# Performance work log

Hardware: AMD Instinct MI355X
Metric: run time of the kernel (lower is better)

Reference implementation:

```python
import jax, jax.numpy as jnp
import numpy as np

N = 4096          # n_nodes
M = 8192          # m_nodes (= 2*N, required by block structure)
D = 128           # in_dim == hidden_dim (conv1 is reapplied to its own output)
H = 128
NUM_ITERS = 3


def setup_inputs() -> dict:
    key = jax.random.key(0)
    ks = jax.random.split(key, 6)
    X = jax.random.normal(ks[0], (N, D), dtype=jnp.float32)
    R = jax.random.uniform(ks[1], (N, N), dtype=jnp.float32)
    A = 0.5 * (R + R.T)  # symmetric, strictly positive connectivity matrix
    # upsample MLP: Linear(n_nodes -> m_nodes - n_nodes), torch weight layout [out, in]
    W_up = jax.random.normal(ks[2], (M - N, N), dtype=jnp.float32) * 0.02
    b_up = jnp.zeros((M - N,), dtype=jnp.float32)
    # GCNConv linear weights stored [in, out]
    W1 = jax.random.normal(ks[3], (D, H), dtype=jnp.float32) * 0.05
    b1 = jnp.zeros((H,), dtype=jnp.float32)
    W2 = jax.random.normal(ks[4], (H, H), dtype=jnp.float32) * 0.05
    b2 = jnp.zeros((H,), dtype=jnp.float32)
    return dict(X=X, A=A, W_up=W_up, b_up=b_up, W1=W1, b1=b1, W2=W2, b2=b2)


def _gcn(Adj, X, W, b):
    # PyG GCNConv on a fully dense, strictly-positive weighted graph:
    # every diagonal entry is nonzero, so add_remaining_self_loops is a no-op and
    # out = D^{-1/2} A D^{-1/2} (X W) + b  exactly.
    deg = Adj.sum(axis=0)                         # [m] column degree
    dinv = jnp.where(deg > 0, jax.lax.rsqrt(deg), 0.0)
    An = Adj * dinv[:, None] * dinv[None, :]      # symmetric normalization
    return An @ (X @ W) + b


def reference(X, A, W_up, b_up, W1, b1, W2, b2):
    # new_nodes = upsample_mlp(X.T).T  -> [M-N, D]
    new_nodes = (X.T @ W_up.T + b_up).T
    Xu = jnp.concatenate([X, new_nodes], axis=0)  # [M, D]
    # block adjacency: [[A, A.T], [A, sigmoid(new @ new.T)]]
    Adj = jnp.block([[A, A.T],
                     [A, jax.nn.sigmoid(new_nodes @ new_nodes.T)]])  # [M, M]
    A_out = Adj
    for _ in range(NUM_ITERS):
        Xu = jax.nn.relu(_gcn(Adj, Xu, W1, b1))
        Adj = jax.nn.sigmoid(Xu @ Xu.T)           # mid-loop adjacency rebuild
        Xu = jax.nn.relu(_gcn(Adj, Xu, W2, b2))
        A_out = jax.nn.sigmoid(Xu @ Xu.T)
        # NOTE: edge_index for the next conv1 is NOT rebuilt from A_out in the
        # original (only after conv1), so Adj carries the mid-loop matrix.
    return A_out
```

## Files before the change

kernel.cpp:

```cpp
#include <hip/hip_runtime.h>
#include <hip/hip_bf16.h>


#define N_NODES 4096
#define M_NODES 8192
#define DIM 128
#define SLICE_ELEMS ((size_t)M_NODES * DIM)

typedef __attribute__((ext_vector_type(4))) float f32x4;
typedef __attribute__((ext_vector_type(8))) short bf16x8;

__device__ __forceinline__ unsigned short f2bf(float f) {
  union { float f; unsigned u; } v; v.f = f;
  unsigned r = v.u + 0x7fffu + ((v.u >> 16) & 1u);
  return (unsigned short)(r >> 16);
}

__device__ __forceinline__ void gld16(unsigned short* lds, const unsigned short* g) {
  __builtin_amdgcn_global_load_lds(
      (const __attribute__((address_space(1))) unsigned int*)g,
      (__attribute__((address_space(3))) unsigned int*)lds, 16, 0, 0);
}

__device__ __forceinline__ float sigmoidf_(float x) { return 1.0f / (1.0f + __expf(-x)); }


__global__ void cast_x_kernel(const float* __restrict__ X, unsigned short* __restrict__ Xu,
                              unsigned short* __restrict__ XT,
                              const float* __restrict__ W1, const float* __restrict__ W2,
                              unsigned short* __restrict__ W1T,
                              unsigned short* __restrict__ W2T,
                              float* __restrict__ deg) {
  int idx = blockIdx.x * 256 + threadIdx.x;
  if (idx < M_NODES) deg[idx] = 0.f;
  if (idx < 32768) {
    const float* W = idx < 16384 ? W1 : W2;
    unsigned short* WT = idx < 16384 ? W1T : W2T;
    int j = idx & 16383;
    int k = j >> 7, c = j & 127;
    WT[c * DIM + k] = f2bf(W[j]);
  }
  int i = idx >> 7, c = idx & 127;
  unsigned short b = f2bf(X[idx]);
  Xu[idx] = b;
  XT[(size_t)c * N_NODES + i] = b;
}

__global__ void cast_a_kernel(const float* __restrict__ A, unsigned short* __restrict__ Adj,
                              float* __restrict__ deg) {
  int c = blockIdx.x * 256 + threadIdx.x;
  int r0 = blockIdx.y * 128;
  int tm = r0 >> 7;
  int kc = c >> 10, st = (c & 1023) >> 5, e = c & 31;
  size_t a1 = ((size_t)(tm)      * 8 + kc)     * 131072 + (size_t)st * 4096 + e;
  size_t a2 = ((size_t)(tm)      * 8 + 4 + kc) * 131072 + (size_t)st * 4096 + e;
  size_t a3 = ((size_t)(tm + 32) * 8 + kc)     * 131072 + (size_t)st * 4096 + e;
  float s = 0.f;
  for (int r = 0; r < 128; ++r) {
    float a = A[(size_t)(r0 + r) * N_NODES + c];
    unsigned short b = f2bf(a);
    Adj[a1 + r * 32] = b; Adj[a2 + r * 32] = b; Adj[a3 + r * 32] = b;
    s += a;
  }
  atomicAdd(&deg[c], 2.0f * s);
  atomicAdd(&deg[N_NODES + c], s);
}


__global__ __launch_bounds__(256, 2)
void agg64_kernel(const unsigned short* __restrict__ At,
                  const unsigned short* __restrict__ BT, long ldb,
                  float* __restrict__ accBase, int kIters) {
  __shared__ __align__(16) unsigned short smem[18432];
  const int t = threadIdx.x, w = t >> 6, lane = t & 63;
  const int q = lane >> 4, l15 = lane & 15;
  const int sx = (l15 >> 1) & 3;
  const int wm = w & 1, wn = w >> 1;
  const int tm = blockIdx.x >> 1;
  const int h2048 = (blockIdx.x & 1) * 2048;
  const int sg0 = blockIdx.y * kIters;
  const int arow = t >> 2;
  const int xchk = (t & 3) ^ ((t >> 3) & 3);

  auto STAGE = [&](int s, int b) {
    unsigned short* la = smem + b * 6144;
    unsigned short* lb = la + 2048;
    int sg = sg0 + s;
    size_t aaddr = ((size_t)tm * 8 + (sg >> 5)) * 131072 + (size_t)(sg & 31) * 4096 + h2048;
    gld16(&la[t * 8],        &At[aaddr + arow * 32 + xchk * 8]);
    gld16(&lb[t * 8],        &BT[(size_t)arow * ldb + (size_t)sg * 32 + xchk * 8]);
    gld16(&lb[2048 + t * 8], &BT[(size_t)(64 + arow) * ldb + (size_t)sg * 32 + xchk * 8]);
  };

  f32x4 acc[2][4];
#pragma unroll
  for (int a = 0; a < 2; ++a)
#pragma unroll
    for (int b = 0; b < 4; ++b) acc[a][b] = (f32x4)0.f;

  STAGE(0, 0);
  STAGE(1, 1);

  for (int s = 0; s < kIters; ++s) {
    if (s + 2 < kIters) {
      STAGE(s + 2, (s + 2) % 3);
      asm volatile("s_waitcnt vmcnt(6)" ::: "memory");
    } else if (s + 1 < kIters) {
      asm volatile("s_waitcnt vmcnt(3)" ::: "memory");
    } else {
      asm volatile("s_waitcnt vmcnt(0)" ::: "memory");
    }
    __builtin_amdgcn_s_barrier();
    __builtin_amdgcn_sched_barrier(0);

    const unsigned short* la = smem + (s % 3) * 6144;
    const unsigned short* lb = la + 2048;
    bf16x8 a0 = *(const bf16x8*)&la[(wm * 32 + l15) * 32 + (q ^ sx) * 8];
    bf16x8 a1 = *(const bf16x8*)&la[(wm * 32 + 16 + l15) * 32 + (q ^ sx) * 8];
#pragma unroll
    for (int nt = 0; nt < 4; ++nt) {
      bf16x8 b = *(const bf16x8*)&lb[(wn * 64 + nt * 16 + l15) * 32 + (q ^ sx) * 8];
      acc[0][nt] = __builtin_amdgcn_mfma_f32_16x16x32_bf16(a0, b, acc[0][nt], 0, 0, 0);
      acc[1][nt] = __builtin_amdgcn_mfma_f32_16x16x32_bf16(a1, b, acc[1][nt], 0, 0, 0);
    }
    __builtin_amdgcn_sched_barrier(0);
    __builtin_amdgcn_s_barrier();
    __builtin_amdgcn_sched_barrier(0);
  }
  float* ct = accBase + (size_t)blockIdx.y * SLICE_ELEMS + (size_t)blockIdx.x * 8192;
#pragma unroll
  for (int mt = 0; mt < 2; ++mt)
#pragma unroll
    for (int nt = 0; nt < 4; ++nt)
      *(f32x4*)&ct[((w * 8 + mt * 4 + nt) * 256) + (q * 16 + l15) * 4] = acc[mt][nt];
}


__global__ __launch_bounds__(256)
void up_agg_f32(const float* __restrict__ Wup, const unsigned short* __restrict__ BT,
                float* __restrict__ accBase) {
  __shared__ __align__(16) unsigned short smem[6144];
  unsigned short* la = smem;
  unsigned short* lb = smem + 2048;
  const int t = threadIdx.x, w = t >> 6, lane = t & 63;
  const int q = lane >> 4, l15 = lane & 15;
  const int r0 = blockIdx.x * 64;
  const int k0 = blockIdx.y * 512;
  const int arow = t >> 2, achk = t & 3;

  f32x4 acc[8];
#pragma unroll
  for (int b = 0; b < 8; ++b) acc[b] = (f32x4)0.f;

  for (int s = 0; s < 16; ++s) {
    int kb = k0 + s * 32;
    __syncthreads();
    gld16(&lb[t * 8],        &BT[(size_t)arow * N_NODES + kb + achk * 8]);
    gld16(&lb[2048 + t * 8], &BT[(size_t)(64 + arow) * N_NODES + kb + achk * 8]);
    const float* ap = &Wup[(size_t)(r0 + (t >> 2)) * N_NODES + kb + (t & 3) * 8];
    float4 v0 = *(const float4*)ap;
    float4 v1 = *(const float4*)(ap + 4);
    ushort4 o0, o1;
    o0.x = f2bf(v0.x); o0.y = f2bf(v0.y); o0.z = f2bf(v0.z); o0.w = f2bf(v0.w);
    o1.x = f2bf(v1.x); o1.y = f2bf(v1.y); o1.z = f2bf(v1.z); o1.w = f2bf(v1.w);
    *(ushort4*)&la[t * 8] = o0;
    *(ushort4*)&la[t * 8 + 4] = o1;
    __syncthreads();

    bf16x8 a0 = *(const bf16x8*)&la[(w * 16 + l15) * 32 + q * 8];
#pragma unroll
    for (int nt = 0; nt < 8; ++nt) {
      bf16x8 b = *(const bf16x8*)&lb[(nt * 16 + l15) * 32 + q * 8];
      acc[nt] = __builtin_amdgcn_mfma_f32_16x16x32_bf16(a0, b, acc[nt], 0, 0, 0);
    }
  }
  float* ct = accBase + (size_t)blockIdx.y * SLICE_ELEMS + (size_t)blockIdx.x * 8192;
#pragma unroll
  for (int nt = 0; nt < 8; ++nt)
    *(f32x4*)&ct[((w * 8 + nt) * 256) + (q * 16 + l15) * 4] = acc[nt];
}

__global__ void reduce64_kernel(const float* __restrict__ acc,
                                unsigned short* __restrict__ dst,
                                const float* __restrict__ bias_row,
                                const float* __restrict__ bias_col,
                                const float* __restrict__ deg, int mode, int nSlices) {
  int p = blockIdx.x * 256 + threadIdx.x;
  float s = 0.f;
  for (int sp = 0; sp < nSlices; ++sp) s += acc[(size_t)sp * SLICE_ELEMS + p];
  int tile = p >> 13, r = p & 8191;
  int grp = r >> 8;
  int r2 = r & 255;
  int i = r2 & 3, ql = r2 >> 2;
  int row, col;
  float v;
  if (mode == 0) {
    int w = grp >> 3, nt = grp & 7;
    row = tile * 64 + w * 16 + (ql >> 4) * 4 + i;
    col = nt * 16 + (ql & 15);
    v = s + bias_row[row];
  } else {
    int w = grp >> 3, mt = (grp >> 2) & 1, nt = grp & 3;
    row = tile * 64 + (w & 1) * 32 + mt * 16 + (ql >> 4) * 4 + i;
    col = (w >> 1) * 64 + nt * 16 + (ql & 15);
    float d = deg[row];
    float dv = d > 0.f ? rsqrtf(d) : 0.f;
    v = fmaxf(dv * s + bias_col[col], 0.f);
  }
  dst[(size_t)row * DIM + col] = f2bf(v);
}


template <int MODE>
__global__ __launch_bounds__(256)
void rebuild_kernel(const unsigned short* __restrict__ XA,
                    const unsigned short* __restrict__ XB,
                    void* __restrict__ out, long p1 ,
                    long col0, float* __restrict__ deg, int nB) {
  __shared__ __align__(16) unsigned short smem[34816];
  __shared__ float lcol[128];
  __shared__ float lrow[128];
  unsigned short* lA = smem;
  unsigned short* lB = smem + 16384;
  const int t = threadIdx.x, w = t >> 6, lane = t & 63;
  const int q = lane >> 4, l15 = lane & 15;
  const int sx = (l15 >> 1) & 3;

  int rem = blockIdx.x, bi = 0;
  while (rem >= nB - bi) { rem -= nB - bi; ++bi; }
  const int bj = bi + rem;
  const int i0 = bi * 128, j0 = bj * 128;
  const bool offdiag = (bi != bj);

  const int srow = t >> 2;
  const int xchk = (t & 3) ^ ((t >> 3) & 3);
#pragma unroll
  for (int kk = 0; kk < 4; ++kk)
#pragma unroll
    for (int h = 0; h < 2; ++h) {
      gld16(&lA[kk * 4096 + h * 2048 + t * 8],
            &XA[(size_t)(i0 + h * 64 + srow) * DIM + kk * 32 + xchk * 8]);
      gld16(&lB[kk * 4096 + h * 2048 + t * 8],
            &XB[(size_t)(j0 + h * 64 + srow) * DIM + kk * 32 + xchk * 8]);
    }
  if (MODE == 0 && t < 128) { lcol[t] = 0.f; lrow[t] = 0.f; }
  __syncthreads();

  f32x4 acc[2][8];
#pragma unroll
  for (int a = 0; a < 2; ++a)
#pragma unroll
    for (int b = 0; b < 8; ++b) acc[a][b] = (f32x4)0.f;

#pragma unroll
  for (int kk = 0; kk < 4; ++kk) {
    bf16x8 a0 = *(const bf16x8*)&lA[kk * 4096 + (w * 32 + l15) * 32 + ((q ^ sx)) * 8];
    bf16x8 a1 = *(const bf16x8*)&lA[kk * 4096 + (w * 32 + 16 + l15) * 32 + ((q ^ sx)) * 8];
#pragma unroll
    for (int nt = 0; nt < 8; ++nt) {
      bf16x8 b = *(const bf16x8*)&lB[kk * 4096 + (nt * 16 + l15) * 32 + ((q ^ sx)) * 8];
      acc[0][nt] = __builtin_amdgcn_mfma_f32_16x16x32_bf16(a0, b, acc[0][nt], 0, 0, 0);
      acc[1][nt] = __builtin_amdgcn_mfma_f32_16x16x32_bf16(a1, b, acc[1][nt], 0, 0, 0);
    }
  }
  __syncthreads();

  if (MODE == 0) {
    unsigned short* lC  = smem;
    unsigned short* lCt = smem + 17408;
    float rs[2][4] = {{0.f, 0.f, 0.f, 0.f}, {0.f, 0.f, 0.f, 0.f}};
#pragma unroll
    for (int mt = 0; mt < 2; ++mt)
#pragma unroll
      for (int nt = 0; nt < 8; ++nt) {
        float cs = 0.f;
#pragma unroll
        for (int i = 0; i < 4; ++i) {
          float sv = sigmoidf_(acc[mt][nt][i]);
          cs += sv;
          unsigned short hb = f2bf(sv);
          int row = w * 32 + mt * 16 + q * 4 + i, colL = nt * 16 + l15;
          lC[row * 136 + colL] = hb;
          if (offdiag) { lCt[colL * 136 + row] = hb; rs[mt][i] += sv; }
        }
        cs += __shfl_xor(cs, 16);
        cs += __shfl_xor(cs, 32);
        if (lane < 16) atomicAdd(&lcol[nt * 16 + lane], cs);
      }
    if (offdiag) {
#pragma unroll
      for (int mt = 0; mt < 2; ++mt)
#pragma unroll
        for (int i = 0; i < 4; ++i) {
          float v = rs[mt][i];
          v += __shfl_xor(v, 1); v += __shfl_xor(v, 2);
          v += __shfl_xor(v, 4); v += __shfl_xor(v, 8);
          if (l15 == 0) atomicAdd(&lrow[w * 32 + mt * 16 + q * 4 + i], v);
        }
    }
    __syncthreads();
    unsigned short* og = (unsigned short*)out;
    {
      const long rowbase = p1 + i0, colbase = col0 + j0;
      const size_t tb = ((size_t)(rowbase >> 7) * 8 + (colbase >> 10)) * 131072;
      const int stb = (int)((colbase & 1023) >> 5);
#pragma unroll
      for (int cc = 0; cc < 8; ++cc) {
        int ch = t + cc * 256;
        int row = ch >> 4, c16 = ch & 15;
        *(bf16x8*)&og[tb + (size_t)(stb + (c16 >> 2)) * 4096 + row * 32 + (c16 & 3) * 8] =
            *(const bf16x8*)&lC[row * 136 + c16 * 8];
      }
    }
    if (offdiag) {
      const long rowbase = p1 + j0, colbase = col0 + i0;
      const size_t tb = ((size_t)(rowbase >> 7) * 8 + (colbase >> 10)) * 131072;
      const int stb = (int)((colbase & 1023) >> 5);
#pragma unroll
      for (int cc = 0; cc < 8; ++cc) {
        int ch = t + cc * 256;
        int row = ch >> 4, c16 = ch & 15;
        *(bf16x8*)&og[tb + (size_t)(stb + (c16 >> 2)) * 4096 + row * 32 + (c16 & 3) * 8] =
            *(const bf16x8*)&lCt[row * 136 + c16 * 8];
      }
    }
    if (t < 128) atomicAdd(&deg[col0 + j0 + t], lcol[t]);
    if (offdiag && t < 128) atomicAdd(&deg[col0 + i0 + t], lrow[t]);
  } else {
    float* og = (float*)out;
    float* lCf = (float*)smem;
#pragma unroll
    for (int mt = 0; mt < 2; ++mt)
#pragma unroll
      for (int nt = 0; nt < 8; ++nt)
#pragma unroll
        for (int i = 0; i < 4; ++i) acc[mt][nt][i] = sigmoidf_(acc[mt][nt][i]);
#pragma unroll
    for (int h2 = 0; h2 < 2; ++h2) {
      __syncthreads();
      if ((w >> 1) == h2) {
#pragma unroll
        for (int mt = 0; mt < 2; ++mt)
#pragma unroll
          for (int nt = 0; nt < 8; ++nt)
#pragma unroll
            for (int i = 0; i < 4; ++i)
              lCf[((w & 1) * 32 + mt * 16 + q * 4 + i) * 132 + nt * 16 + l15] =
                  acc[mt][nt][i];
      }
      __syncthreads();
#pragma unroll
      for (int j = 0; j < 8; ++j) {
        int ch = t + j * 256;
        int r64 = ch >> 5, c4 = (ch & 31) * 4;
        *(f32x4*)&og[(size_t)(i0 + h2 * 64 + r64) * p1 + j0 + c4] =
            *(const f32x4*)&lCf[r64 * 132 + c4];
      }
    }
    if (offdiag) {
#pragma unroll
      for (int h2 = 0; h2 < 2; ++h2) {
        __syncthreads();
#pragma unroll
        for (int mt = 0; mt < 2; ++mt)
#pragma unroll
          for (int nt = 0; nt < 8; ++nt)
            if ((nt >> 2) == h2) {
#pragma unroll
              for (int i = 0; i < 4; ++i)
                lCf[((nt & 3) * 16 + l15) * 132 + (w * 32 + mt * 16 + q * 4 + i)] =
                    acc[mt][nt][i];
            }
        __syncthreads();
#pragma unroll
        for (int j = 0; j < 8; ++j) {
          int ch = t + j * 256;
          int r64 = ch >> 5, c4 = (ch & 31) * 4;
          *(f32x4*)&og[(size_t)(j0 + h2 * 64 + r64) * p1 + i0 + c4] =
              *(const f32x4*)&lCf[r64 * 132 + c4];
        }
      }
    }
  }
}


__global__ __launch_bounds__(256)
void yz_kernel(const unsigned short* __restrict__ Xu, const unsigned short* __restrict__ WT,
               const float* __restrict__ deg, unsigned short* __restrict__ ZT, int ldz,
               float* __restrict__ zbuf) {
  __shared__ __align__(16) unsigned short smem[32768];
  unsigned short* lA = smem;
  unsigned short* lB = smem + 16384;
  const int t = threadIdx.x, w = t >> 6, lane = t & 63;
  const int q = lane >> 4, l15 = lane & 15;
  const int sx = (l15 >> 1) & 3;
  const int r0 = blockIdx.x * 128;
  if (zbuf) {
    int gid = blockIdx.x * 256 + t;
    if (gid < M_NODES) zbuf[gid] = 0.f;
  }
  const int srow = t >> 2;
  const int xchk = (t & 3) ^ ((t >> 3) & 3);
#pragma unroll
  for (int kk = 0; kk < 4; ++kk)
#pragma unroll
    for (int h = 0; h < 2; ++h) {
      gld16(&lA[kk * 4096 + h * 2048 + t * 8],
            &Xu[(size_t)(r0 + h * 64 + srow) * DIM + kk * 32 + xchk * 8]);
      gld16(&lB[kk * 4096 + h * 2048 + t * 8],
            &WT[(size_t)(h * 64 + srow) * DIM + kk * 32 + xchk * 8]);
    }
  __syncthreads();

  f32x4 acc[2][8];
#pragma unroll
  for (int a = 0; a < 2; ++a)
#pragma unroll
    for (int b = 0; b < 8; ++b) acc[a][b] = (f32x4)0.f;

#pragma unroll
  for (int kk = 0; kk < 4; ++kk) {
    bf16x8 a0 = *(const bf16x8*)&lA[kk * 4096 + (w * 32 + l15) * 32 + (q ^ sx) * 8];
    bf16x8 a1 = *(const bf16x8*)&lA[kk * 4096 + (w * 32 + 16 + l15) * 32 + (q ^ sx) * 8];
#pragma unroll
    for (int nt = 0; nt < 8; ++nt) {
      bf16x8 b = *(const bf16x8*)&lB[kk * 4096 + (nt * 16 + l15) * 32 + (q ^ sx) * 8];
      acc[0][nt] = __builtin_amdgcn_mfma_f32_16x16x32_bf16(a0, b, acc[0][nt], 0, 0, 0);
      acc[1][nt] = __builtin_amdgcn_mfma_f32_16x16x32_bf16(a1, b, acc[1][nt], 0, 0, 0);
    }
  }
  __syncthreads();
  unsigned short* lT = smem;
#pragma unroll
  for (int mt = 0; mt < 2; ++mt)
#pragma unroll
    for (int i = 0; i < 4; ++i) {
      int r = w * 32 + mt * 16 + q * 4 + i;
      float d = deg[r0 + r];
      float dv = d > 0.f ? rsqrtf(d) : 0.f;
#pragma unroll
      for (int nt = 0; nt < 8; ++nt)
        lT[(nt * 16 + l15) * 136 + r] = f2bf(dv * acc[mt][nt][i]);
    }
  __syncthreads();
#pragma unroll
  for (int cc = 0; cc < 8; ++cc) {
    int ch = t + cc * 256;
    int c = ch >> 4, c16 = ch & 15;
    *(bf16x8*)&ZT[(size_t)c * ldz + r0 + c16 * 8] = *(const bf16x8*)&lT[c * 136 + c16 * 8];
  }
}


extern "C" void kernel_launch(void* const* d_in, const int* in_sizes, int n_in,
                              void* d_out, int out_size, void* d_ws, size_t ws_size,
                              hipStream_t stream) {
  (void)in_sizes; (void)n_in; (void)out_size;
  const float* X   = (const float*)d_in[0];
  const float* A   = (const float*)d_in[1];
  const float* Wup = (const float*)d_in[2];
  const float* bup = (const float*)d_in[3];
  const float* W1  = (const float*)d_in[4];
  const float* b1  = (const float*)d_in[5];
  const float* W2  = (const float*)d_in[6];
  const float* b2  = (const float*)d_in[7];

  const size_t ADJ_BYTES = (size_t)M_NODES * M_NODES * 2;
  char* ws = (char*)d_ws;
  size_t off = 0;
  auto alloc = [&](size_t bytes) {
    char* p = ws + off;
    off += (bytes + 255) & ~(size_t)255;
    return p;
  };
  float*          accb    = (float*)alloc(8 * SLICE_ELEMS * 4);
  unsigned short* Xu      = (unsigned short*)alloc((size_t)M_NODES * DIM * 2);
  unsigned short* ZT      = (unsigned short*)alloc((size_t)DIM * M_NODES * 2);
  unsigned short* XT      = (unsigned short*)alloc((size_t)DIM * N_NODES * 2);
  unsigned short* W1T     = (unsigned short*)alloc(DIM * DIM * 2);
  unsigned short* W2T     = (unsigned short*)alloc(DIM * DIM * 2);
  float*          degA    = (float*)alloc(M_NODES * 4);
  float*          degB    = (float*)alloc(M_NODES * 4);

  unsigned short* Adj;
  if (ws_size >= off + ADJ_BYTES) Adj = (unsigned short*)(ws + off);
  else                            Adj = (unsigned short*)d_out;

  unsigned short* XuNew = Xu + (size_t)N_NODES * DIM;

  cast_x_kernel<<<N_NODES * DIM / 256, 256, 0, stream>>>(X, Xu, XT, W1, W2, W1T, W2T, degA);

  up_agg_f32<<<dim3(N_NODES / 64, 8), 256, 0, stream>>>(Wup, XT, accb);
  reduce64_kernel<<<N_NODES * DIM / 256, 256, 0, stream>>>(
      accb, XuNew, bup, nullptr, nullptr, 0, 8);

  cast_a_kernel<<<dim3(N_NODES / 256, N_NODES / 128), 256, 0, stream>>>(A, Adj, degA);
  rebuild_kernel<0><<<32 * 33 / 2, 256, 0, stream>>>(
      XuNew, XuNew, Adj, N_NODES, N_NODES, degA, 32);

  float* degCur = degA;
  float* degMid = degB;
  for (int it = 0; it < 3; ++it) {
    yz_kernel<<<M_NODES / 128, 256, 0, stream>>>(Xu, W1T, degCur, ZT, M_NODES, degMid);
    agg64_kernel<<<dim3(M_NODES / 64, 4), 256, 0, stream>>>(Adj, ZT, M_NODES, accb, 64);
    reduce64_kernel<<<M_NODES * DIM / 256, 256, 0, stream>>>(
        accb, Xu, nullptr, b1, degCur, 1, 4);
    rebuild_kernel<0><<<64 * 65 / 2, 256, 0, stream>>>(
        Xu, Xu, Adj, 0, 0, degMid, 64);
    yz_kernel<<<M_NODES / 128, 256, 0, stream>>>(Xu, W2T, degMid, ZT, M_NODES, nullptr);
    agg64_kernel<<<dim3(M_NODES / 64, 4), 256, 0, stream>>>(Adj, ZT, M_NODES, accb, 64);
    reduce64_kernel<<<M_NODES * DIM / 256, 256, 0, stream>>>(
        accb, Xu, nullptr, b2, degMid, 1, 4);
    if (it == 2)
      rebuild_kernel<1><<<64 * 65 / 2, 256, 0, stream>>>(
          Xu, Xu, d_out, M_NODES, 0, nullptr, 64);
    float* tmp = degCur; degCur = degMid; degMid = tmp;
  }
}
```

Before: 893.7 us.

## Store adjacency as 8-bit e5m2 and aggregate with f16 MFMA

The 8192x8192 adjacency is stored as 1-byte e5m2 (truncated fp16) instead of bf16, halving its memory footprint and traffic in the rebuild and aggregation kernels. The aggregation kernel is rewritten to load 64-wide K chunks of fp8 A, expand them to fp16 in registers with byte permutes, and feed f16 MFMAs, with ZT now produced in fp16. Degree sums are computed from the quantized values so the normalization stays consistent with them. The cost is a large precision drop for adjacency values (2 mantissa bits), which risks accuracy tolerance, plus extra ALU work to expand the bytes.

```diff
diff --git a/kernel.cpp b/kernel.cpp
--- a/kernel.cpp
+++ b/kernel.cpp
@@ -9,6 +9,7 @@
 
 typedef __attribute__((ext_vector_type(4))) float f32x4;
 typedef __attribute__((ext_vector_type(8))) short bf16x8;
+typedef __attribute__((ext_vector_type(8))) _Float16 half8;
 
 __device__ __forceinline__ unsigned short f2bf(float f) {
   union { float f; unsigned u; } v; v.f = f;
@@ -16,13 +17,44 @@
   return (unsigned short)(r >> 16);
 }
 
+__device__ __forceinline__ unsigned short f2h(float f) {
+  union { _Float16 h; unsigned short u; } v; v.h = (_Float16)f; return v.u;
+}
+
+__device__ __forceinline__ unsigned char f2e5(float f) {
+  unsigned short h = f2h(f);
+  unsigned short r = h + 0x7Fu + ((h >> 8) & 1u);
+  return (unsigned char)(r >> 8);
+}
+__device__ __forceinline__ float e5tof(unsigned char b) {
+  union { unsigned short u; _Float16 h; } v; v.u = (unsigned short)b << 8;
+  return (float)v.h;
+}
+
 __device__ __forceinline__ void gld16(unsigned short* lds, const unsigned short* g) {
   __builtin_amdgcn_global_load_lds(
       (const __attribute__((address_space(1))) unsigned int*)g,
       (__attribute__((address_space(3))) unsigned int*)lds, 16, 0, 0);
 }
+__device__ __forceinline__ void gld16b(unsigned char* lds, const unsigned char* g) {
+  __builtin_amdgcn_global_load_lds(
+      (const __attribute__((address_space(1))) unsigned int*)g,
+      (__attribute__((address_space(3))) unsigned int*)lds, 16, 0, 0);
+}
 
 __device__ __forceinline__ float sigmoidf_(float x) { return 1.0f / (1.0f + __expf(-x)); }
+
+__device__ __forceinline__ half8 expandA(const unsigned char* la, int row, int c16, int hf) {
+  const unsigned* p =
+      (const unsigned*)&la[(((c16 ^ (row & 3)) * 64 + row) * 16) + hf * 8];
+  unsigned x0 = p[0], x1 = p[1];
+  union { unsigned u[4]; half8 h; } r;
+  r.u[0] = __builtin_amdgcn_perm(x0, 0u, 0x050C040Cu);
+  r.u[1] = __builtin_amdgcn_perm(x0, 0u, 0x070C060Cu);
+  r.u[2] = __builtin_amdgcn_perm(x1, 0u, 0x050C040Cu);
+  r.u[3] = __builtin_amdgcn_perm(x1, 0u, 0x070C060Cu);
+  return r.h;
+}
 
 
 __global__ void cast_x_kernel(const float* __restrict__ X, unsigned short* __restrict__ Xu,
@@ -46,7 +78,7 @@
   XT[(size_t)c * N_NODES + i] = b;
 }
 
-__global__ void cast_a_kernel(const float* __restrict__ A, unsigned short* __restrict__ Adj,
+__global__ void cast_a_kernel(const float* __restrict__ A, unsigned char* __restrict__ Adj,
                               float* __restrict__ deg) {
   int c = blockIdx.x * 256 + threadIdx.x;
   int r0 = blockIdx.y * 128;
@@ -58,9 +90,9 @@
   float s = 0.f;
   for (int r = 0; r < 128; ++r) {
     float a = A[(size_t)(r0 + r) * N_NODES + c];
-    unsigned short b = f2bf(a);
+    unsigned char b = f2e5(a);
     Adj[a1 + r * 32] = b; Adj[a2 + r * 32] = b; Adj[a3 + r * 32] = b;
-    s += a;
+    s += e5tof(b);
   }
   atomicAdd(&deg[c], 2.0f * s);
   atomicAdd(&deg[N_NODES + c], s);
@@ -68,28 +100,34 @@
 
 
 __global__ __launch_bounds__(256, 2)
-void agg64_kernel(const unsigned short* __restrict__ At,
+void aggf8_kernel(const unsigned char* __restrict__ At,
                   const unsigned short* __restrict__ BT, long ldb,
-                  float* __restrict__ accBase, int kIters) {
-  __shared__ __align__(16) unsigned short smem[18432];
+                  float* __restrict__ accBase) {
+  __shared__ __align__(16) unsigned char smem[61440];
   const int t = threadIdx.x, w = t >> 6, lane = t & 63;
   const int q = lane >> 4, l15 = lane & 15;
-  const int sx = (l15 >> 1) & 3;
   const int wm = w & 1, wn = w >> 1;
   const int tm = blockIdx.x >> 1;
-  const int h2048 = (blockIdx.x & 1) * 2048;
-  const int sg0 = blockIdx.y * kIters;
-  const int arow = t >> 2;
-  const int xchk = (t & 3) ^ ((t >> 3) & 3);
+  const int hrow = (blockIdx.x & 1) * 64;
+  const int sg0 = blockIdx.y * 64;
+  const int arow = lane;
+  const int ac16 = w ^ (lane & 3);
 
   auto STAGE = [&](int s, int b) {
-    unsigned short* la = smem + b * 6144;
-    unsigned short* lb = la + 2048;
-    int sg = sg0 + s;
-    size_t aaddr = ((size_t)tm * 8 + (sg >> 5)) * 131072 + (size_t)(sg & 31) * 4096 + h2048;
-    gld16(&la[t * 8],        &At[aaddr + arow * 32 + xchk * 8]);
-    gld16(&lb[t * 8],        &BT[(size_t)arow * ldb + (size_t)sg * 32 + xchk * 8]);
-    gld16(&lb[2048 + t * 8], &BT[(size_t)(64 + arow) * ldb + (size_t)sg * 32 + xchk * 8]);
+    unsigned char* la = smem + b * 20480;
+    unsigned short* lb = (unsigned short*)(la + 4096);
+    int sg = sg0 + 2 * s + (ac16 >> 1);
+    gld16b(&la[t * 16],
+           &At[((size_t)tm * 8 + (sg >> 5)) * 131072 + (size_t)(sg & 31) * 4096 +
+               (hrow + arow) * 32 + (ac16 & 1) * 16]);
+    size_t kb = (size_t)sg0 * 32 + (size_t)s * 64;
+#pragma unroll
+    for (int j = 0; j < 4; ++j) {
+      int ch = j * 256 + t;
+      int row = ch >> 3, phys = ch & 7;
+      int c = phys ^ (row & 7);
+      gld16(&lb[ch * 8], &BT[(size_t)row * ldb + kb + c * 8]);
+    }
   };
 
   f32x4 acc[2][4];
@@ -101,27 +139,33 @@
   STAGE(0, 0);
   STAGE(1, 1);
 
-  for (int s = 0; s < kIters; ++s) {
-    if (s + 2 < kIters) {
+  for (int s = 0; s < 32; ++s) {
+    if (s + 2 < 32) {
       STAGE(s + 2, (s + 2) % 3);
-      asm volatile("s_waitcnt vmcnt(6)" ::: "memory");
-    } else if (s + 1 < kIters) {
-      asm volatile("s_waitcnt vmcnt(3)" ::: "memory");
+      asm volatile("s_waitcnt vmcnt(10)" ::: "memory");
+    } else if (s + 1 < 32) {
+      asm volatile("s_waitcnt vmcnt(5)" ::: "memory");
     } else {
       asm volatile("s_waitcnt vmcnt(0)" ::: "memory");
     }
     __builtin_amdgcn_s_barrier();
     __builtin_amdgcn_sched_barrier(0);
 
-    const unsigned short* la = smem + (s % 3) * 6144;
-    const unsigned short* lb = la + 2048;
-    bf16x8 a0 = *(const bf16x8*)&la[(wm * 32 + l15) * 32 + (q ^ sx) * 8];
-    bf16x8 a1 = *(const bf16x8*)&la[(wm * 32 + 16 + l15) * 32 + (q ^ sx) * 8];
-#pragma unroll
-    for (int nt = 0; nt < 4; ++nt) {
-      bf16x8 b = *(const bf16x8*)&lb[(wn * 64 + nt * 16 + l15) * 32 + (q ^ sx) * 8];
-      acc[0][nt] = __builtin_amdgcn_mfma_f32_16x16x32_bf16(a0, b, acc[0][nt], 0, 0, 0);
-      acc[1][nt] = __builtin_amdgcn_mfma_f32_16x16x32_bf16(a1, b, acc[1][nt], 0, 0, 0);
+    const unsigned char* la = smem + (s % 3) * 20480;
+    const unsigned short* lb = (const unsigned short*)(la + 4096);
+#pragma unroll
+    for (int kk = 0; kk < 2; ++kk) {
+      int ch8 = kk * 4 + q;
+      int c16 = ch8 >> 1, hf = ch8 & 1;
+      half8 a0 = expandA(la, wm * 32 + l15, c16, hf);
+      half8 a1 = expandA(la, wm * 32 + 16 + l15, c16, hf);
+#pragma unroll
+      for (int nt = 0; nt < 4; ++nt) {
+        int brow = wn * 64 + nt * 16 + l15;
+        half8 b = *(const half8*)&lb[brow * 64 + (ch8 ^ (l15 & 7)) * 8];
+        acc[0][nt] = __builtin_amdgcn_mfma_f32_16x16x32_f16(a0, b, acc[0][nt], 0, 0, 0);
+        acc[1][nt] = __builtin_amdgcn_mfma_f32_16x16x32_f16(a1, b, acc[1][nt], 0, 0, 0);
+      }
     }
     __builtin_amdgcn_sched_barrier(0);
     __builtin_amdgcn_s_barrier();
@@ -266,8 +310,8 @@
   __syncthreads();
 
   if (MODE == 0) {
-    unsigned short* lC  = smem;
-    unsigned short* lCt = smem + 17408;
+    unsigned char* lC  = (unsigned char*)smem;
+    unsigned char* lCt = (unsigned char*)smem + 17408;
     float rs[2][4] = {{0.f, 0.f, 0.f, 0.f}, {0.f, 0.f, 0.f, 0.f}};
 #pragma unroll
     for (int mt = 0; mt < 2; ++mt)
@@ -276,12 +320,12 @@
         float cs = 0.f;
 #pragma unroll
         for (int i = 0; i < 4; ++i) {
-          float sv = sigmoidf_(acc[mt][nt][i]);
-          cs += sv;
-          unsigned short hb = f2bf(sv);
+          unsigned char hb = f2e5(sigmoidf_(acc[mt][nt][i]));
+          float dq = e5tof(hb);
+          cs += dq;
           int row = w * 32 + mt * 16 + q * 4 + i, colL = nt * 16 + l15;
           lC[row * 136 + colL] = hb;
-          if (offdiag) { lCt[colL * 136 + row] = hb; rs[mt][i] += sv; }
+          if (offdiag) { lCt[colL * 136 + row] = hb; rs[mt][i] += dq; }
         }
         cs += __shfl_xor(cs, 16);
         cs += __shfl_xor(cs, 32);
@@ -299,7 +343,7 @@
         }
     }
     __syncthreads();
-    unsigned short* og = (unsigned short*)out;
+    unsigned char* og = (unsigned char*)out;
     {
       const long rowbase = p1 + i0, colbase = col0 + j0;
       const size_t tb = ((size_t)(rowbase >> 7) * 8 + (colbase >> 10)) * 131072;
@@ -308,8 +352,9 @@
       for (int cc = 0; cc < 8; ++cc) {
         int ch = t + cc * 256;
         int row = ch >> 4, c16 = ch & 15;
-        *(bf16x8*)&og[tb + (size_t)(stb + (c16 >> 2)) * 4096 + row * 32 + (c16 & 3) * 8] =
-            *(const bf16x8*)&lC[row * 136 + c16 * 8];
+        *(unsigned long long*)
+            &og[tb + (size_t)(stb + (c16 >> 2)) * 4096 + row * 32 + (c16 & 3) * 8] =
+            *(const unsigned long long*)&lC[row * 136 + c16 * 8];
       }
     }
     if (offdiag) {
@@ -320,8 +365,9 @@
       for (int cc = 0; cc < 8; ++cc) {
         int ch = t + cc * 256;
         int row = ch >> 4, c16 = ch & 15;
-        *(bf16x8*)&og[tb + (size_t)(stb + (c16 >> 2)) * 4096 + row * 32 + (c16 & 3) * 8] =
-            *(const bf16x8*)&lCt[row * 136 + c16 * 8];
+        *(unsigned long long*)
+            &og[tb + (size_t)(stb + (c16 >> 2)) * 4096 + row * 32 + (c16 & 3) * 8] =
+            *(const unsigned long long*)&lCt[row * 136 + c16 * 8];
       }
     }
     if (t < 128) atomicAdd(&deg[col0 + j0 + t], lcol[t]);
@@ -441,7 +487,7 @@
       float dv = d > 0.f ? rsqrtf(d) : 0.f;
 #pragma unroll
       for (int nt = 0; nt < 8; ++nt)
-        lT[(nt * 16 + l15) * 136 + r] = f2bf(dv * acc[mt][nt][i]);
+        lT[(nt * 16 + l15) * 136 + r] = f2h(dv * acc[mt][nt][i]);
     }
   __syncthreads();
 #pragma unroll
@@ -466,7 +512,7 @@
   const float* W2  = (const float*)d_in[6];
   const float* b2  = (const float*)d_in[7];
 
-  const size_t ADJ_BYTES = (size_t)M_NODES * M_NODES * 2;
+  const size_t ADJ_BYTES = (size_t)M_NODES * M_NODES;
   char* ws = (char*)d_ws;
   size_t off = 0;
   auto alloc = [&](size_t bytes) {
@@ -483,9 +529,9 @@
   float*          degA    = (float*)alloc(M_NODES * 4);
   float*          degB    = (float*)alloc(M_NODES * 4);
 
-  unsigned short* Adj;
-  if (ws_size >= off + ADJ_BYTES) Adj = (unsigned short*)(ws + off);
-  else                            Adj = (unsigned short*)d_out;
+  unsigned char* Adj;
+  if (ws_size >= off + ADJ_BYTES) Adj = (unsigned char*)(ws + off);
+  else                            Adj = (unsigned char*)d_out;
 
   unsigned short* XuNew = Xu + (size_t)N_NODES * DIM;
 
@@ -503,13 +549,13 @@
   float* degMid = degB;
   for (int it = 0; it < 3; ++it) {
     yz_kernel<<<M_NODES / 128, 256, 0, stream>>>(Xu, W1T, degCur, ZT, M_NODES, degMid);
-    agg64_kernel<<<dim3(M_NODES / 64, 4), 256, 0, stream>>>(Adj, ZT, M_NODES, accb, 64);
+    aggf8_kernel<<<dim3(M_NODES / 64, 4), 256, 0, stream>>>(Adj, ZT, M_NODES, accb);
     reduce64_kernel<<<M_NODES * DIM / 256, 256, 0, stream>>>(
         accb, Xu, nullptr, b1, degCur, 1, 4);
     rebuild_kernel<0><<<64 * 65 / 2, 256, 0, stream>>>(
         Xu, Xu, Adj, 0, 0, degMid, 64);
     yz_kernel<<<M_NODES / 128, 256, 0, stream>>>(Xu, W2T, degMid, ZT, M_NODES, nullptr);
-    agg64_kernel<<<dim3(M_NODES / 64, 4), 256, 0, stream>>>(Adj, ZT, M_NODES, accb, 64);
+    aggf8_kernel<<<dim3(M_NODES / 64, 4), 256, 0, stream>>>(Adj, ZT, M_NODES, accb);
     reduce64_kernel<<<M_NODES * DIM / 256, 256, 0, stream>>>(
         accb, Xu, nullptr, b2, degMid, 1, 4);
     if (it == 2)
```

Measured after the change: 834.1 us, median of 2. 6.7% less time.
